# Optimization experiments

Measured on AMD Instinct MI355X. Metric: run time of the kernel, lower is better.

## Reference

```python
import jax, jax.numpy as jnp
import numpy as np

NUM_HEADS = 32
KV_HEADS = 8
HEAD_DIM = 128
ROPE_BASE = 10000.0

def apply_rope(x):
    # x: [B, H, S, D]
    B, H, S, D = x.shape
    inv_freq = 1.0 / (ROPE_BASE ** (jnp.arange(0, D, 2, dtype=jnp.float32) / D))  # [D/2]
    t = jnp.arange(S, dtype=jnp.float32)
    freqs = jnp.einsum('s,d->sd', t, inv_freq)                 # [S, D/2]
    emb = jnp.concatenate([freqs, freqs], axis=-1)             # [S, D]
    cos = jnp.cos(emb)[None, None, :, :].astype(x.dtype)
    sin = jnp.sin(emb)[None, None, :, :].astype(x.dtype)
    x1, x2 = x[..., : D // 2], x[..., D // 2 :]
    rotated = jnp.concatenate([-x2, x1], axis=-1)
    return x * cos + rotated * sin

def setup_inputs() -> dict:
    key = jax.random.key(0)
    ks = jax.random.split(key, 6)
    B, S, H = 1, 2048, 4096
    scale = 1.0 / np.sqrt(H)
    return {
        'hidden_states': jax.random.normal(ks[0], (B, S, H), jnp.float32),
        'attention_mask': jnp.zeros((B, S), jnp.float32),
        'Wq': jax.random.normal(ks[1], (H, NUM_HEADS * HEAD_DIM), jnp.float32) * scale,
        'Wk': jax.random.normal(ks[2], (H, KV_HEADS * HEAD_DIM), jnp.float32) * scale,
        'Wv': jax.random.normal(ks[3], (H, KV_HEADS * HEAD_DIM), jnp.float32) * scale,
        'Wo': jax.random.normal(ks[4], (NUM_HEADS * HEAD_DIM, H), jnp.float32) * scale,
    }

def reference(hidden_states, attention_mask, Wq, Wk, Wv, Wo):
    B, S, _ = hidden_states.shape
    groups = NUM_HEADS // KV_HEADS
    q = (hidden_states @ Wq).reshape(B, S, NUM_HEADS, HEAD_DIM).transpose(0, 2, 1, 3)  # [B,H,S,D]
    k = (hidden_states @ Wk).reshape(B, S, KV_HEADS, HEAD_DIM).transpose(0, 2, 1, 3)   # [B,KV,S,D]
    v = (hidden_states @ Wv).reshape(B, S, KV_HEADS, HEAD_DIM).transpose(0, 2, 1, 3)
    q = apply_rope(q)
    k = apply_rope(k)
    # GQA: repeat kv heads to match query heads
    k = jnp.repeat(k, groups, axis=1)  # [B,H,S,D]
    v = jnp.repeat(v, groups, axis=1)
    scale = 1.0 / jnp.sqrt(jnp.asarray(HEAD_DIM, q.dtype))
    scores = jnp.einsum('bhqd,bhkd->bhqk', q, k) * scale       # [B,H,S,S]
    scores = scores + attention_mask[:, None, None, :]
    attn = jax.nn.softmax(scores, axis=-1)
    out = jnp.einsum('bhqk,bhkd->bhqd', attn, v)               # [B,H,S,D]
    out = out.transpose(0, 2, 1, 3).reshape(B, S, NUM_HEADS * HEAD_DIM)
    return out @ Wo
```

## Files before the change

kernel.cpp:

```cpp
#include <hip/hip_runtime.h>
#include <hip/hip_bf16.h>

typedef __bf16 bf16_t;
typedef __bf16 bf16x8 __attribute__((ext_vector_type(8)));
typedef __bf16 bf16x4 __attribute__((ext_vector_type(4)));
typedef float f32x4 __attribute__((ext_vector_type(4)));
typedef float f32x16 __attribute__((ext_vector_type(16)));

__device__ __forceinline__ void gload_lds16(const void* g, void* l) {
  __builtin_amdgcn_global_load_lds((const __attribute__((address_space(1))) void*)g,
                                   (__attribute__((address_space(3))) void*)l, 16, 0, 0);
}

__device__ __forceinline__ unsigned pk_bf16(float a, float b) {
  unsigned r;
  asm("v_cvt_pk_bf16_f32 %0, %1, %2" : "=v"(r) : "v"(a), "v"(b));
  return r;
}

__global__ __launch_bounds__(256) void cvt_bf16_kernel(const float* __restrict__ src,
                                                       bf16_t* __restrict__ dst, int n8) {
  int i = blockIdx.x * 256 + threadIdx.x;
  if (i >= n8) return;
  const float4* s4 = (const float4*)src;
  float4 a = s4[2 * i], b = s4[2 * i + 1];
  bf16x8 o;
  o[0] = (bf16_t)a.x; o[1] = (bf16_t)a.y; o[2] = (bf16_t)a.z; o[3] = (bf16_t)a.w;
  o[4] = (bf16_t)b.x; o[5] = (bf16_t)b.y; o[6] = (bf16_t)b.z; o[7] = (bf16_t)b.w;
  *(bf16x8*)(dst + 8 * (size_t)i) = o;
}

__global__ __launch_bounds__(256) void trcvt_kernel(const float* __restrict__ src,
                                                    bf16_t* __restrict__ dst, int R, int C) {
  __shared__ float tile[32][33];
  int c0 = blockIdx.x * 32, r0 = blockIdx.y * 32;
  int tx = threadIdx.x, ty = threadIdx.y;
#pragma unroll
  for (int i = 0; i < 4; ++i)
    tile[ty + i * 8][tx] = src[(size_t)(r0 + ty + i * 8) * C + c0 + tx];
  __syncthreads();
#pragma unroll
  for (int i = 0; i < 4; ++i)
    dst[(size_t)(c0 + ty + i * 8) * R + r0 + tx] = (bf16_t)tile[tx][ty + i * 8];
}

__global__ __launch_bounds__(256) void trcvt_perm_kernel(const float* __restrict__ src,
                                                         bf16_t* __restrict__ dst, int R, int C) {
  __shared__ float tile[32][33];
  int c0 = blockIdx.x * 32, r0 = blockIdx.y * 32;
  int tx = threadIdx.x, ty = threadIdx.y;
#pragma unroll
  for (int i = 0; i < 4; ++i)
    tile[ty + i * 8][tx] = src[(size_t)(r0 + ty + i * 8) * C + c0 + tx];
  __syncthreads();
#pragma unroll
  for (int i = 0; i < 4; ++i) {
    int rc = c0 + ty + i * 8;
    int dd = rc & 127;
    int q = (dd & 15) + ((dd & 16)) + ((dd >> 5) & 1 ? 64 : 0) + ((dd >> 6) ? 32 : 0);
    int r_out = (rc & ~127) | q;
    dst[(size_t)r_out * R + r0 + tx] = (bf16_t)tile[tx][ty + i * 8];
  }
}

__global__ __launch_bounds__(256) void trb_kernel(const bf16_t* __restrict__ src,
                                                  bf16_t* __restrict__ dst, int R, int C) {
  __shared__ bf16_t tile[32][33];
  int c0 = blockIdx.x * 32, r0 = blockIdx.y * 32;
  int tx = threadIdx.x, ty = threadIdx.y;
#pragma unroll
  for (int i = 0; i < 4; ++i)
    tile[ty + i * 8][tx] = src[(size_t)(r0 + ty + i * 8) * C + c0 + tx];
  __syncthreads();
#pragma unroll
  for (int i = 0; i < 4; ++i)
    dst[(size_t)(c0 + ty + i * 8) * R + r0 + tx] = tile[tx][ty + i * 8];
}

__global__ __launch_bounds__(256) void rope_tab_kernel(float* __restrict__ cosT,
                                                       float* __restrict__ sinT) {
  int i = blockIdx.x * 256 + threadIdx.x;
  int s = i >> 6, d = i & 63;
  float ang = (float)s * powf(10000.0f, -(float)d * (1.0f / 64.0f));
  cosT[i] = cosf(ang);
  sinT[i] = sinf(ang);
}

__global__ __launch_bounds__(512, 2) void proj_gemm_kernel(
    const bf16_t* __restrict__ A, const bf16_t* __restrict__ Wqt,
    const bf16_t* __restrict__ Wkvt, const float* __restrict__ cosT,
    const float* __restrict__ sinT, bf16_t* __restrict__ Qb,
    bf16_t* __restrict__ Kb, bf16_t* __restrict__ Vb) {
  constexpr int K = 4096;
  extern __shared__ unsigned char sMem[];
  const int bx = blockIdx.x;
  const int mt = bx & 7, nt = bx >> 3;
  const int bm = mt * 256;
  const bf16_t* Btb = (nt < 16) ? (Wqt + (size_t)nt * 256 * K)
                                : (Wkvt + (size_t)(nt - 16) * 256 * K);

  const int t = threadIdx.x;
  const int rowU = t >> 2;
  const int cole = ((t & 3) * 8) ^ ((rowU & 8) ? 16 : 0);
  const bf16_t* aS = A + (size_t)(bm + rowU) * K + cole;
  const bf16_t* bS = Btb + (size_t)rowU * K + cole;

  const int lane = t & 63, w = t >> 6;
  const int wm = w >> 2, wn = w & 3;
  const int lr = lane & 15, lq = lane >> 4;
  const int colb = (lq * 16) ^ ((lr & 8) ? 32 : 0);

  auto stA = [&](int c, int h, int j) {
    unsigned char* d = sMem + c * 65536 + h * 16384 + t * 16;
    const bf16_t* g = aS + (size_t)h * 128 * K + j * 64;
    gload_lds16(g, d);
    gload_lds16(g + 32, d + 8192);
  };
  auto stB = [&](int c, int h, int j) {
    unsigned char* d = sMem + c * 65536 + 32768 + h * 16384 + t * 16;
    const bf16_t* g = bS + (size_t)h * 128 * K + j * 64;
    gload_lds16(g, d);
    gload_lds16(g + 32, d + 8192);
  };
  auto LA = [&](int c, int half, int mi, int kk) {
    return *(const bf16x8*)(sMem + c * 65536 + wm * 16384 + kk * 8192 +
                            (half * 64 + mi * 16 + lr) * 64 + colb);
  };
  auto LB = [&](int c, int ni, int kk) {
    return *(const bf16x8*)(sMem + c * 65536 + 32768 + (wn >> 1) * 16384 + kk * 8192 +
                            ((wn & 1) * 64 + ni * 16 + lr) * 64 + colb);
  };

  f32x4 acc[8][4];
#pragma unroll
  for (int i = 0; i < 8; ++i)
#pragma unroll
    for (int n = 0; n < 4; ++n) acc[i][n] = f32x4{0.f, 0.f, 0.f, 0.f};

  stA(0, 0, 0); stA(0, 1, 0); stB(0, 0, 0); stB(0, 1, 0);
  stB(1, 0, 1); stB(1, 1, 1);
  asm volatile("s_waitcnt vmcnt(4)" ::: "memory");
  __builtin_amdgcn_s_barrier();
  __builtin_amdgcn_sched_barrier(0);

  bf16x8 af[4][2], bf[2][2], bf2[2][2];
  for (int j = 0; j < 64; ++j) {
    const int c = j & 1, cn = c ^ 1;
    const int jp1 = (j + 1 < 64) ? j + 1 : 63;
    const int jp2 = (j + 2 < 64) ? j + 2 : 63;
#pragma unroll
    for (int mi = 0; mi < 4; ++mi)
#pragma unroll
      for (int kk = 0; kk < 2; ++kk) af[mi][kk] = LA(c, 0, mi, kk);
#pragma unroll
    for (int ni = 0; ni < 2; ++ni)
#pragma unroll
      for (int kk = 0; kk < 2; ++kk) bf[ni][kk] = LB(c, ni, kk);
    stA(cn, 0, jp1);
    __builtin_amdgcn_s_barrier();
    __builtin_amdgcn_sched_barrier(0);
    __builtin_amdgcn_s_setprio(1);
#pragma unroll
    for (int kk = 0; kk < 2; ++kk)
#pragma unroll
      for (int mi = 0; mi < 4; ++mi)
#pragma unroll
        for (int ni = 0; ni < 2; ++ni)
          acc[mi][ni] = __builtin_amdgcn_mfma_f32_16x16x32_bf16(af[mi][kk], bf[ni][kk],
                                                                acc[mi][ni], 0, 0, 0);
    __builtin_amdgcn_s_setprio(0);
    __builtin_amdgcn_sched_barrier(0);
    __builtin_amdgcn_s_barrier();
#pragma unroll
    for (int ni = 0; ni < 2; ++ni)
#pragma unroll
      for (int kk = 0; kk < 2; ++kk) bf2[ni][kk] = LB(c, 2 + ni, kk);
    stA(cn, 1, jp1);
    __builtin_amdgcn_s_barrier();
    __builtin_amdgcn_sched_barrier(0);
    __builtin_amdgcn_s_setprio(1);
#pragma unroll
    for (int kk = 0; kk < 2; ++kk)
#pragma unroll
      for (int mi = 0; mi < 4; ++mi)
#pragma unroll
        for (int ni = 0; ni < 2; ++ni)
          acc[mi][2 + ni] = __builtin_amdgcn_mfma_f32_16x16x32_bf16(af[mi][kk], bf2[ni][kk],
                                                                    acc[mi][2 + ni], 0, 0, 0);
    __builtin_amdgcn_s_setprio(0);
    __builtin_amdgcn_sched_barrier(0);
    __builtin_amdgcn_s_barrier();
#pragma unroll
    for (int mi = 0; mi < 4; ++mi)
#pragma unroll
      for (int kk = 0; kk < 2; ++kk) af[mi][kk] = LA(c, 1, mi, kk);
    stB(c, 0, jp2);
    __builtin_amdgcn_s_barrier();
    __builtin_amdgcn_sched_barrier(0);
    __builtin_amdgcn_s_setprio(1);
#pragma unroll
    for (int kk = 0; kk < 2; ++kk)
#pragma unroll
      for (int mi = 0; mi < 4; ++mi)
#pragma unroll
        for (int ni = 0; ni < 2; ++ni)
          acc[4 + mi][2 + ni] = __builtin_amdgcn_mfma_f32_16x16x32_bf16(
              af[mi][kk], bf2[ni][kk], acc[4 + mi][2 + ni], 0, 0, 0);
    __builtin_amdgcn_s_setprio(0);
    __builtin_amdgcn_sched_barrier(0);
    __builtin_amdgcn_s_barrier();
    stB(c, 1, jp2);
    asm volatile("s_waitcnt vmcnt(4)" ::: "memory");
    __builtin_amdgcn_s_barrier();
    __builtin_amdgcn_sched_barrier(0);
    __builtin_amdgcn_s_setprio(1);
#pragma unroll
    for (int kk = 0; kk < 2; ++kk)
#pragma unroll
      for (int mi = 0; mi < 4; ++mi)
#pragma unroll
        for (int ni = 0; ni < 2; ++ni)
          acc[4 + mi][ni] = __builtin_amdgcn_mfma_f32_16x16x32_bf16(
              af[mi][kk], bf[ni][kk], acc[4 + mi][ni], 0, 0, 0);
    __builtin_amdgcn_s_setprio(0);
    __builtin_amdgcn_sched_barrier(0);
    __builtin_amdgcn_s_barrier();
  }

  if (nt < 20) {
    const bool isQ = nt < 16;
    bf16_t* dst = isQ ? Qb : Kb;
    const int ld = isQ ? 4096 : 1024;
    const int hh = isQ ? (nt * 2 + (wn >> 1)) : ((nt - 16) * 2 + (wn >> 1));
    const float qs = isQ ? 0.08838834764831845f : 1.0f;
    const int dbase = lr + 32 * (wn & 1);
#pragma unroll
    for (int half = 0; half < 2; ++half)
#pragma unroll
      for (int mi = 0; mi < 4; ++mi)
#pragma unroll
        for (int ni = 0; ni < 2; ++ni) {
          int d = dbase + 16 * ni;
#pragma unroll
          for (int r = 0; r < 4; ++r) {
            int srow = bm + wm * 128 + half * 64 + mi * 16 + lq * 4 + r;
            float cv = cosT[srow * 64 + d], sv = sinT[srow * 64 + d];
            float x1 = acc[half * 4 + mi][ni][r], x2 = acc[half * 4 + mi][ni + 2][r];
            dst[(size_t)srow * ld + hh * 128 + d] = (bf16_t)((x1 * cv - x2 * sv) * qs);
            dst[(size_t)srow * ld + hh * 128 + d + 64] = (bf16_t)((x2 * cv + x1 * sv) * qs);
          }
        }
  } else {
    const int col0 = (nt - 20) * 256 + wn * 64;
#pragma unroll
    for (int half = 0; half < 2; ++half)
#pragma unroll
      for (int mi = 0; mi < 4; ++mi)
#pragma unroll
        for (int ni = 0; ni < 4; ++ni)
#pragma unroll
          for (int r = 0; r < 4; ++r) {
            int srow = bm + wm * 128 + half * 64 + mi * 16 + lq * 4 + r;
            Vb[(size_t)srow * 1024 + col0 + ni * 16 + lr] =
                (bf16_t)acc[half * 4 + mi][ni][r];
          }
  }
}

__global__ __launch_bounds__(256, 2) void out_gemm_kernel(
    const bf16_t* __restrict__ A, const bf16_t* __restrict__ B0,
    float* __restrict__ Cout) {
  constexpr int K = 4096;
  constexpr int MT = 16;
  __shared__ alignas(16) unsigned char sAB[32768];
  unsigned char* sA = sAB;
  unsigned char* sB = sAB + 16384;
  const int bx = blockIdx.x;
  const int mt = bx % MT, nt = bx / MT;
  const int bm = mt * 128;
  const bf16_t* Bt = B0 + (size_t)nt * 128 * K;

  const int t = threadIdx.x;
  const int sr = t >> 3;
  const int scol = ((t & 7) ^ (sr & 7)) * 8;
  const bf16_t* aG = A + (size_t)(bm + sr) * K + scol;
  const bf16_t* bG = Bt + (size_t)sr * K + scol;
  unsigned char* aL = sA + t * 16;
  unsigned char* bL = sB + t * 16;

  const int lane = t & 63, w = t >> 6;
  const int lr = lane & 15, lq = lane >> 4;
  const int swz = (lr & 7) << 4;

  f32x4 acc[2][8];
#pragma unroll
  for (int m = 0; m < 2; ++m)
#pragma unroll
    for (int n = 0; n < 8; ++n) acc[m][n] = f32x4{0.f, 0.f, 0.f, 0.f};

  for (int k0 = 0; k0 < K; k0 += 64) {
    __syncthreads();
#pragma unroll
    for (int p = 0; p < 4; ++p) {
      gload_lds16(aG + (size_t)(p * 32) * K + k0, aL + p * 4096);
      gload_lds16(bG + (size_t)(p * 32) * K + k0, bL + p * 4096);
    }
    __syncthreads();
#pragma unroll
    for (int kk = 0; kk < 2; ++kk) {
      bf16x8 af[2], bfr[8];
#pragma unroll
      for (int m = 0; m < 2; ++m)
        af[m] = *(const bf16x8*)(sA + (w * 32 + m * 16 + lr) * 128 +
                                 ((kk * 64 + lq * 16) ^ swz));
#pragma unroll
      for (int n = 0; n < 8; ++n)
        bfr[n] = *(const bf16x8*)(sB + (n * 16 + lr) * 128 +
                                  ((kk * 64 + lq * 16) ^ swz));
#pragma unroll
      for (int m = 0; m < 2; ++m)
#pragma unroll
        for (int n = 0; n < 8; ++n)
          acc[m][n] = __builtin_amdgcn_mfma_f32_16x16x32_bf16(af[m], bfr[n],
                                                              acc[m][n], 0, 0, 0);
    }
  }
#pragma unroll
  for (int m = 0; m < 2; ++m)
#pragma unroll
    for (int n = 0; n < 8; ++n)
#pragma unroll
      for (int r = 0; r < 4; ++r)
        Cout[(size_t)(bm + w * 32 + m * 16 + lq * 4 + r) * 4096 + nt * 128 +
             n * 16 + lr] = acc[m][n][r];
}

__global__ __launch_bounds__(512) void attn_kernel(
    const bf16_t* __restrict__ Qb, const bf16_t* __restrict__ Kb,
    const bf16_t* __restrict__ Vt, const float* __restrict__ mask,
    bf16_t* __restrict__ Ob) {
  extern __shared__ unsigned char sMem[];
  const int bx = blockIdx.x;
  const int h = bx >> 3, qt = bx & 7;
  const int kvh = h >> 2;
  const int t = threadIdx.x, lane = t & 63, w = t >> 6;
  const int ln = lane & 31, hi = lane >> 5;
  const int q0 = qt * 256 + w * 32;
  const int swz = (ln & 7) << 4;

  bf16x8 qf[8];
#pragma unroll
  for (int ds = 0; ds < 8; ++ds)
    qf[ds] = *(const bf16x8*)(Qb + (size_t)(q0 + ln) * 4096 + h * 128 + ds * 16 + hi * 8);

  const int krow = t >> 4, kg = t & 15;
  const bf16_t* kSrc = Kb + (size_t)krow * 1024 + kvh * 128 +
                       (((kg * 16) ^ ((krow & 7) << 4)) >> 1);
  const int vrow = t >> 3, vg = t & 7;
  const bf16_t* vSrc = Vt + (size_t)(kvh * 128 + vrow) * 2048 +
                       (((vg * 16) ^ ((vrow & 7) << 4)) >> 1);

  auto stage = [&](int c, int kt) {
    unsigned char* kD = sMem + c * 16384 + t * 16;
    unsigned char* vD = sMem + 32768 + c * 16384 + t * 16;
    gload_lds16(kSrc + (size_t)kt * 64 * 1024, kD);
    gload_lds16(kSrc + (size_t)(kt * 64 + 32) * 1024, kD + 8192);
    gload_lds16(vSrc + kt * 64, vD);
    gload_lds16(vSrc + (size_t)64 * 2048 + kt * 64, vD + 8192);
    if (t < 16) gload_lds16(mask + kt * 64 + t * 4, sMem + 65536 + c * 256 + t * 16);
  };

  f32x16 o[4];
#pragma unroll
  for (int db = 0; db < 4; ++db)
#pragma unroll
    for (int e = 0; e < 16; ++e) o[db][e] = 0.f;
  float mrun = -1e30f, lp = 0.f;

  stage(0, 0);
  __syncthreads();

  for (int kt = 0; kt < 32; ++kt) {
    const int c = kt & 1;
    if (kt < 31) stage(c ^ 1, kt + 1);
    const unsigned char* sK = sMem + c * 16384;
    const unsigned char* sV = sMem + 32768 + c * 16384;
    const unsigned char* sMk = sMem + 65536 + c * 256;

#pragma unroll
    for (int sub = 0; sub < 2; ++sub) {
      f32x16 s;
#pragma unroll
      for (int e = 0; e < 16; ++e) s[e] = 0.f;
      __builtin_amdgcn_s_setprio(1);
#pragma unroll
      for (int ds = 0; ds < 8; ++ds) {
        bf16x8 kf = *(const bf16x8*)(sK + (sub * 32 + ln) * 256 +
                                     ((ds * 32 + hi * 16) ^ swz));
        s = __builtin_amdgcn_mfma_f32_32x32x16_bf16(kf, qf[ds], s, 0, 0, 0);
      }
      __builtin_amdgcn_s_setprio(0);
#pragma unroll
      for (int rg = 0; rg < 4; ++rg) {
        float4 mv = *(const float4*)(sMk + (sub * 32 + rg * 8 + 4 * hi) * 4);
        s[rg * 4 + 0] += mv.x; s[rg * 4 + 1] += mv.y;
        s[rg * 4 + 2] += mv.z; s[rg * 4 + 3] += mv.w;
      }
      float pm = s[0];
#pragma unroll
      for (int e = 1; e < 16; ++e) pm = fmaxf(pm, s[e]);
      pm = fmaxf(pm, __shfl_xor(pm, 32));
      if (!__all(pm - mrun <= 8.0f)) {
        float nm = fmaxf(mrun, pm);
        float al = __expf(mrun - nm);
        mrun = nm;
        lp *= al;
#pragma unroll
        for (int db = 0; db < 4; ++db)
#pragma unroll
          for (int e = 0; e < 16; ++e) o[db][e] *= al;
      }
      float p[16], ps = 0.f;
#pragma unroll
      for (int e = 0; e < 16; ++e) {
        p[e] = __expf(s[e] - mrun);
        ps += p[e];
      }
      lp += ps;
#pragma unroll
      for (int hh = 0; hh < 2; ++hh) {
        unsigned w0 = pk_bf16(p[8 * hh + 0], p[8 * hh + 1]);
        unsigned w1 = pk_bf16(p[8 * hh + 2], p[8 * hh + 3]);
        unsigned w2 = pk_bf16(p[8 * hh + 4], p[8 * hh + 5]);
        unsigned w3 = pk_bf16(p[8 * hh + 6], p[8 * hh + 7]);
        unsigned pw0 = __shfl_xor((int)w0, 32), pw1 = __shfl_xor((int)w1, 32);
        unsigned pw2 = __shfl_xor((int)w2, 32), pw3 = __shfl_xor((int)w3, 32);
        union { unsigned u[4]; bf16x8 v; } pf;
        pf.u[0] = hi ? pw2 : w0;
        pf.u[1] = hi ? pw3 : w1;
        pf.u[2] = hi ? w2 : pw0;
        pf.u[3] = hi ? w3 : pw1;
        __builtin_amdgcn_s_setprio(1);
#pragma unroll
        for (int db = 0; db < 4; ++db) {
          bf16x8 vf = *(const bf16x8*)(sV + (db * 32 + ln) * 128 +
                                       ((sub * 64 + hh * 32 + hi * 16) ^ swz));
          o[db] = __builtin_amdgcn_mfma_f32_32x32x16_bf16(vf, pf.v, o[db], 0, 0, 0);
        }
        __builtin_amdgcn_s_setprio(0);
      }
    }
    __syncthreads();
  }

  float l = lp + __shfl_xor(lp, 32);
  float inv = 1.0f / l;
  bf16_t* orow = Ob + (size_t)(q0 + ln) * 4096 + h * 128;
#pragma unroll
  for (int db = 0; db < 4; ++db)
#pragma unroll
    for (int rg = 0; rg < 4; ++rg) {
      bf16x4 ov;
#pragma unroll
      for (int j = 0; j < 4; ++j) ov[j] = (bf16_t)(o[db][rg * 4 + j] * inv);
      *(bf16x4*)(orow + db * 32 + rg * 8 + hi * 4) = ov;
    }
}

extern "C" void kernel_launch(void* const* d_in, const int* in_sizes, int n_in,
                              void* d_out, int out_size, void* d_ws, size_t ws_size,
                              hipStream_t stream) {
  const float* hidden = (const float*)d_in[0];
  const float* mask = (const float*)d_in[1];
  const float* Wq = (const float*)d_in[2];
  const float* Wk = (const float*)d_in[3];
  const float* Wv = (const float*)d_in[4];
  const float* Wo = (const float*)d_in[5];
  float* out = (float*)d_out;
  char* ws = (char*)d_ws;

  bf16_t* hB   = (bf16_t*)(ws + 0);
  bf16_t* Wqt  = (bf16_t*)(ws + 16777216);
  bf16_t* Wkvt = (bf16_t*)(ws + 50331648);
  bf16_t* Wot  = (bf16_t*)(ws + 67108864);
  bf16_t* Qb   = (bf16_t*)(ws + 100663296);
  bf16_t* Kb   = (bf16_t*)(ws + 117440512);
  bf16_t* Vb   = (bf16_t*)(ws + 121634816);
  bf16_t* Vt   = (bf16_t*)(ws + 125829120);
  bf16_t* Ob   = (bf16_t*)(ws + 130023424);
  float*  cosT = (float*)(ws + 146800640);
  float*  sinT = (float*)(ws + 147324928);

  hipFuncSetAttribute((const void*)attn_kernel,
                      hipFuncAttributeMaxDynamicSharedMemorySize, 66560);
  hipFuncSetAttribute((const void*)proj_gemm_kernel,
                      hipFuncAttributeMaxDynamicSharedMemorySize, 131072);

  cvt_bf16_kernel<<<4096, 256, 0, stream>>>(hidden, hB, 1048576);
  trcvt_perm_kernel<<<dim3(128, 128), dim3(32, 8), 0, stream>>>(Wq, Wqt, 4096, 4096);
  trcvt_perm_kernel<<<dim3(32, 128), dim3(32, 8), 0, stream>>>(Wk, Wkvt, 4096, 1024);
  trcvt_kernel<<<dim3(32, 128), dim3(32, 8), 0, stream>>>(Wv, Wkvt + (size_t)1024 * 4096, 4096, 1024);
  trcvt_kernel<<<dim3(128, 128), dim3(32, 8), 0, stream>>>(Wo, Wot, 4096, 4096);
  rope_tab_kernel<<<512, 256, 0, stream>>>(cosT, sinT);
  proj_gemm_kernel<<<192, 512, 131072, stream>>>(hB, Wqt, Wkvt, cosT, sinT, Qb, Kb, Vb);
  trb_kernel<<<dim3(32, 64), dim3(32, 8), 0, stream>>>(Vb, Vt, 2048, 1024);
  attn_kernel<<<256, 512, 66560, stream>>>(Qb, Kb, Vt, mask, Ob);
  out_gemm_kernel<<<512, 256, 0, stream>>>(Ob, Wot, out);
}
```

Measured before the change: 329.2 us.

## Fuse prep kernels, retile attention to 256-thread blocks, use exp2 softmax

Merges the hidden-state conversion, rope table and four weight transpose-convert launches into one large prep kernel to cut launch overhead and tail gaps. Splits attention into 512 blocks of 256 threads covering 128 queries each, with two blocks per CU, and folds log2e into the Q scale so softmax uses exp2. Also moves the projection GEMM's vmcnt wait past the MFMA block and drops one barrier, which risks a race if the LDS stage is not yet complete.

Result: no change. 333.8 us (+1.4%).

```diff
diff --git a/kernel.cpp b/kernel.cpp
--- a/kernel.cpp
+++ b/kernel.cpp
@@ -7,6 +7,8 @@
 typedef float f32x4 __attribute__((ext_vector_type(4)));
 typedef float f32x16 __attribute__((ext_vector_type(16)));
 
+#define LOG2E 1.4426950408889634f
+
 __device__ __forceinline__ void gload_lds16(const void* g, void* l) {
   __builtin_amdgcn_global_load_lds((const __attribute__((address_space(1))) void*)g,
                                    (__attribute__((address_space(3))) void*)l, 16, 0, 0);
@@ -18,48 +20,64 @@
   return r;
 }
 
-__global__ __launch_bounds__(256) void cvt_bf16_kernel(const float* __restrict__ src,
-                                                       bf16_t* __restrict__ dst, int n8) {
-  int i = blockIdx.x * 256 + threadIdx.x;
-  if (i >= n8) return;
-  const float4* s4 = (const float4*)src;
-  float4 a = s4[2 * i], b = s4[2 * i + 1];
-  bf16x8 o;
-  o[0] = (bf16_t)a.x; o[1] = (bf16_t)a.y; o[2] = (bf16_t)a.z; o[3] = (bf16_t)a.w;
-  o[4] = (bf16_t)b.x; o[5] = (bf16_t)b.y; o[6] = (bf16_t)b.z; o[7] = (bf16_t)b.w;
-  *(bf16x8*)(dst + 8 * (size_t)i) = o;
-}
-
-__global__ __launch_bounds__(256) void trcvt_kernel(const float* __restrict__ src,
-                                                    bf16_t* __restrict__ dst, int R, int C) {
-  __shared__ float tile[32][33];
-  int c0 = blockIdx.x * 32, r0 = blockIdx.y * 32;
-  int tx = threadIdx.x, ty = threadIdx.y;
+__device__ __forceinline__ void trcvt_body(const float* src, bf16_t* dst, int R,
+                                           int C, int cx, int cy, int tx, int ty,
+                                           float (*tile)[33], bool perm) {
+  int c0 = cx * 32, r0 = cy * 32;
 #pragma unroll
   for (int i = 0; i < 4; ++i)
     tile[ty + i * 8][tx] = src[(size_t)(r0 + ty + i * 8) * C + c0 + tx];
   __syncthreads();
 #pragma unroll
-  for (int i = 0; i < 4; ++i)
-    dst[(size_t)(c0 + ty + i * 8) * R + r0 + tx] = (bf16_t)tile[tx][ty + i * 8];
-}
-
-__global__ __launch_bounds__(256) void trcvt_perm_kernel(const float* __restrict__ src,
-                                                         bf16_t* __restrict__ dst, int R, int C) {
-  __shared__ float tile[32][33];
-  int c0 = blockIdx.x * 32, r0 = blockIdx.y * 32;
-  int tx = threadIdx.x, ty = threadIdx.y;
-#pragma unroll
-  for (int i = 0; i < 4; ++i)
-    tile[ty + i * 8][tx] = src[(size_t)(r0 + ty + i * 8) * C + c0 + tx];
-  __syncthreads();
-#pragma unroll
   for (int i = 0; i < 4; ++i) {
     int rc = c0 + ty + i * 8;
-    int dd = rc & 127;
-    int q = (dd & 15) + ((dd & 16)) + ((dd >> 5) & 1 ? 64 : 0) + ((dd >> 6) ? 32 : 0);
-    int r_out = (rc & ~127) | q;
+    int r_out = rc;
+    if (perm) {
+      int dd = rc & 127;
+      int q = (dd & 15) + (dd & 16) + (((dd >> 5) & 1) ? 64 : 0) + ((dd >> 6) ? 32 : 0);
+      r_out = (rc & ~127) | q;
+    }
     dst[(size_t)r_out * R + r0 + tx] = (bf16_t)tile[tx][ty + i * 8];
+  }
+}
+
+__global__ __launch_bounds__(256) void prep_kernel(
+    const float* __restrict__ hidden, const float* __restrict__ Wq,
+    const float* __restrict__ Wk, const float* __restrict__ Wv,
+    const float* __restrict__ Wo, bf16_t* __restrict__ hB,
+    bf16_t* __restrict__ Wqt, bf16_t* __restrict__ Wkvt,
+    bf16_t* __restrict__ Wot, float* __restrict__ cosT,
+    float* __restrict__ sinT) {
+  __shared__ float tile[32][33];
+  const int bx = blockIdx.x;
+  const int t = threadIdx.x;
+  const int tx = t & 31, ty = t >> 5;
+  if (bx < 4096) {
+    int i = bx * 256 + t;
+    const float4* s4 = (const float4*)hidden;
+    float4 a = s4[2 * i], b = s4[2 * i + 1];
+    bf16x8 o;
+    o[0] = (bf16_t)a.x; o[1] = (bf16_t)a.y; o[2] = (bf16_t)a.z; o[3] = (bf16_t)a.w;
+    o[4] = (bf16_t)b.x; o[5] = (bf16_t)b.y; o[6] = (bf16_t)b.z; o[7] = (bf16_t)b.w;
+    *(bf16x8*)(hB + 8 * (size_t)i) = o;
+  } else if (bx < 4608) {
+    int i = (bx - 4096) * 256 + t;
+    int s = i >> 6, d = i & 63;
+    float ang = (float)s * powf(10000.0f, -(float)d * (1.0f / 64.0f));
+    cosT[i] = cosf(ang);
+    sinT[i] = sinf(ang);
+  } else if (bx < 20992) {
+    int j = bx - 4608;
+    trcvt_body(Wq, Wqt, 4096, 4096, j % 128, j / 128, tx, ty, tile, true);
+  } else if (bx < 25088) {
+    int j = bx - 20992;
+    trcvt_body(Wk, Wkvt, 4096, 1024, j % 32, j / 32, tx, ty, tile, true);
+  } else if (bx < 29184) {
+    int j = bx - 25088;
+    trcvt_body(Wv, Wkvt + (size_t)1024 * 4096, 4096, 1024, j % 32, j / 32, tx, ty, tile, false);
+  } else {
+    int j = bx - 29184;
+    trcvt_body(Wo, Wot, 4096, 4096, j % 128, j / 128, tx, ty, tile, false);
   }
 }
 
@@ -75,15 +93,6 @@
 #pragma unroll
   for (int i = 0; i < 4; ++i)
     dst[(size_t)(c0 + ty + i * 8) * R + r0 + tx] = tile[tx][ty + i * 8];
-}
-
-__global__ __launch_bounds__(256) void rope_tab_kernel(float* __restrict__ cosT,
-                                                       float* __restrict__ sinT) {
-  int i = blockIdx.x * 256 + threadIdx.x;
-  int s = i >> 6, d = i & 63;
-  float ang = (float)s * powf(10000.0f, -(float)d * (1.0f / 64.0f));
-  cosT[i] = cosf(ang);
-  sinT[i] = sinf(ang);
 }
 
 __global__ __launch_bounds__(512, 2) void proj_gemm_kernel(
@@ -210,8 +219,6 @@
     __builtin_amdgcn_sched_barrier(0);
     __builtin_amdgcn_s_barrier();
     stB(c, 1, jp2);
-    asm volatile("s_waitcnt vmcnt(4)" ::: "memory");
-    __builtin_amdgcn_s_barrier();
     __builtin_amdgcn_sched_barrier(0);
     __builtin_amdgcn_s_setprio(1);
 #pragma unroll
@@ -223,6 +230,7 @@
           acc[4 + mi][ni] = __builtin_amdgcn_mfma_f32_16x16x32_bf16(
               af[mi][kk], bf[ni][kk], acc[4 + mi][ni], 0, 0, 0);
     __builtin_amdgcn_s_setprio(0);
+    asm volatile("s_waitcnt vmcnt(4)" ::: "memory");
     __builtin_amdgcn_sched_barrier(0);
     __builtin_amdgcn_s_barrier();
   }
@@ -232,7 +240,7 @@
     bf16_t* dst = isQ ? Qb : Kb;
     const int ld = isQ ? 4096 : 1024;
     const int hh = isQ ? (nt * 2 + (wn >> 1)) : ((nt - 16) * 2 + (wn >> 1));
-    const float qs = isQ ? 0.08838834764831845f : 1.0f;
+    const float qs = isQ ? 0.12751743f : 1.0f;
     const int dbase = lr + 32 * (wn & 1);
 #pragma unroll
     for (int half = 0; half < 2; ++half)
@@ -335,17 +343,17 @@
              n * 16 + lr] = acc[m][n][r];
 }
 
-__global__ __launch_bounds__(512) void attn_kernel(
+__global__ __launch_bounds__(256, 2) void attn_kernel(
     const bf16_t* __restrict__ Qb, const bf16_t* __restrict__ Kb,
     const bf16_t* __restrict__ Vt, const float* __restrict__ mask,
     bf16_t* __restrict__ Ob) {
   extern __shared__ unsigned char sMem[];
   const int bx = blockIdx.x;
-  const int h = bx >> 3, qt = bx & 7;
+  const int h = bx >> 4, qt = bx & 15;
   const int kvh = h >> 2;
   const int t = threadIdx.x, lane = t & 63, w = t >> 6;
   const int ln = lane & 31, hi = lane >> 5;
-  const int q0 = qt * 256 + w * 32;
+  const int q0 = qt * 128 + w * 32;
   const int swz = (ln & 7) << 4;
 
   bf16x8 qf[8];
@@ -363,10 +371,12 @@
   auto stage = [&](int c, int kt) {
     unsigned char* kD = sMem + c * 16384 + t * 16;
     unsigned char* vD = sMem + 32768 + c * 16384 + t * 16;
-    gload_lds16(kSrc + (size_t)kt * 64 * 1024, kD);
-    gload_lds16(kSrc + (size_t)(kt * 64 + 32) * 1024, kD + 8192);
-    gload_lds16(vSrc + kt * 64, vD);
-    gload_lds16(vSrc + (size_t)64 * 2048 + kt * 64, vD + 8192);
+#pragma unroll
+    for (int p = 0; p < 4; ++p)
+      gload_lds16(kSrc + (size_t)(kt * 64 + p * 16) * 1024, kD + p * 4096);
+#pragma unroll
+    for (int p = 0; p < 4; ++p)
+      gload_lds16(vSrc + (size_t)(p * 32) * 2048 + kt * 64, vD + p * 4096);
     if (t < 16) gload_lds16(mask + kt * 64 + t * 4, sMem + 65536 + c * 256 + t * 16);
   };
 
@@ -403,16 +413,16 @@
 #pragma unroll
       for (int rg = 0; rg < 4; ++rg) {
         float4 mv = *(const float4*)(sMk + (sub * 32 + rg * 8 + 4 * hi) * 4);
-        s[rg * 4 + 0] += mv.x; s[rg * 4 + 1] += mv.y;
-        s[rg * 4 + 2] += mv.z; s[rg * 4 + 3] += mv.w;
+        s[rg * 4 + 0] += LOG2E * mv.x; s[rg * 4 + 1] += LOG2E * mv.y;
+        s[rg * 4 + 2] += LOG2E * mv.z; s[rg * 4 + 3] += LOG2E * mv.w;
       }
       float pm = s[0];
 #pragma unroll
       for (int e = 1; e < 16; ++e) pm = fmaxf(pm, s[e]);
       pm = fmaxf(pm, __shfl_xor(pm, 32));
-      if (!__all(pm - mrun <= 8.0f)) {
+      if (!__all(pm - mrun <= 11.5f)) {
         float nm = fmaxf(mrun, pm);
-        float al = __expf(mrun - nm);
+        float al = exp2f(mrun - nm);
         mrun = nm;
         lp *= al;
 #pragma unroll
@@ -423,7 +433,7 @@
       float p[16], ps = 0.f;
 #pragma unroll
       for (int e = 0; e < 16; ++e) {
-        p[e] = __expf(s[e] - mrun);
+        p[e] = exp2f(s[e] - mrun);
         ps += p[e];
       }
       lp += ps;
@@ -496,14 +506,10 @@
   hipFuncSetAttribute((const void*)proj_gemm_kernel,
                       hipFuncAttributeMaxDynamicSharedMemorySize, 131072);
 
-  cvt_bf16_kernel<<<4096, 256, 0, stream>>>(hidden, hB, 1048576);
-  trcvt_perm_kernel<<<dim3(128, 128), dim3(32, 8), 0, stream>>>(Wq, Wqt, 4096, 4096);
-  trcvt_perm_kernel<<<dim3(32, 128), dim3(32, 8), 0, stream>>>(Wk, Wkvt, 4096, 1024);
-  trcvt_kernel<<<dim3(32, 128), dim3(32, 8), 0, stream>>>(Wv, Wkvt + (size_t)1024 * 4096, 4096, 1024);
-  trcvt_kernel<<<dim3(128, 128), dim3(32, 8), 0, stream>>>(Wo, Wot, 4096, 4096);
-  rope_tab_kernel<<<512, 256, 0, stream>>>(cosT, sinT);
+  prep_kernel<<<45568, 256, 0, stream>>>(hidden, Wq, Wk, Wv, Wo, hB, Wqt, Wkvt,
+                                         Wot, cosT, sinT);
   proj_gemm_kernel<<<192, 512, 131072, stream>>>(hB, Wqt, Wkvt, cosT, sinT, Qb, Kb, Vb);
   trb_kernel<<<dim3(32, 64), dim3(32, 8), 0, stream>>>(Vb, Vt, 2048, 1024);
-  attn_kernel<<<256, 512, 66560, stream>>>(Qb, Kb, Vt, mask, Ob);
+  attn_kernel<<<512, 256, 66560, stream>>>(Qb, Kb, Vt, mask, Ob);
   out_gemm_kernel<<<512, 256, 0, stream>>>(Ob, Wot, out);
 }
```
